# Optimization experiments

Hardware: AMD Instinct MI355X
Metric: run time of the kernel (lower is better)

Reference implementation:

```python
import jax, jax.numpy as jnp
import numpy as np

EMBED_DIM = 1024
NUM_HEADS = 16
HEAD_DIM = EMBED_DIM // NUM_HEADS
ROPE_BASE = 10000.0
NEG_INF = -1e9


def _rope_tables(T, dim, dtype=jnp.float32):
    inv_freq = 1.0 / (ROPE_BASE ** (jnp.arange(0, dim, 2, dtype=jnp.float32) / dim))
    t = jnp.arange(T, dtype=jnp.float32)
    freqs = jnp.einsum('t,f->tf', t, inv_freq)          # [T, dim/2]
    emb = jnp.concatenate([freqs, freqs], axis=-1)       # [T, dim]
    return jnp.cos(emb).astype(dtype), jnp.sin(emb).astype(dtype)


def _rotate_half(x):
    x1, x2 = jnp.split(x, 2, axis=-1)
    return jnp.concatenate([-x2, x1], axis=-1)


def setup_inputs() -> dict:
    key = jax.random.key(0)
    kx, kqkv, kout = jax.random.split(key, 3)
    B, T = 2, 2048
    x = jax.random.normal(kx, (B, T, EMBED_DIM), dtype=jnp.float32)
    # Dense kernels (no bias), glorot-ish scale
    w_qkv = jax.random.normal(kqkv, (EMBED_DIM, 3 * EMBED_DIM), dtype=jnp.float32) * (EMBED_DIM ** -0.5)
    w_out = jax.random.normal(kout, (EMBED_DIM, EMBED_DIM), dtype=jnp.float32) * (EMBED_DIM ** -0.5)
    return {"x": x, "w_qkv": w_qkv, "w_out": w_out}


def reference(x, w_qkv, w_out):
    B, T, _ = x.shape
    qkv = x @ w_qkv                                      # [B, T, 3E]
    q, k, v = jnp.split(qkv, 3, axis=-1)

    def split_heads(t):
        return t.reshape(B, T, NUM_HEADS, HEAD_DIM).transpose(0, 2, 1, 3)  # [B,H,T,D]

    q, k, v = split_heads(q), split_heads(k), split_heads(v)

    cos, sin = _rope_tables(T, HEAD_DIM, x.dtype)        # [T, D]
    cos = cos[None, None, :, :]
    sin = sin[None, None, :, :]
    q = q * cos + _rotate_half(q) * sin
    k = k * cos + _rotate_half(k) * sin

    scale = jnp.sqrt(jnp.asarray(HEAD_DIM, dtype=jnp.float32)).astype(x.dtype)
    scores = jnp.einsum('bhqd,bhkd->bhqk', q, k) / scale  # [B,H,T,T]
    causal = jnp.tril(jnp.ones((T, T), dtype=bool))[None, None, :, :]
    scores = jnp.where(causal, scores, jnp.asarray(NEG_INF, dtype=x.dtype))
    probs = jax.nn.softmax(scores, axis=-1)
    out = jnp.einsum('bhqk,bhkd->bhqd', probs, v)         # [B,H,T,D]
    out = out.transpose(0, 2, 1, 3).reshape(B, T, EMBED_DIM)
    return out @ w_out
```

## Files before the change

kernel.cpp:

```cpp
#include <hip/hip_runtime.h>
#include <hip/hip_bf16.h>
#include <cstdint>

#define DI __device__ __forceinline__

using u16x8  = __attribute__((ext_vector_type(8))) unsigned short;
using u32x4  = __attribute__((ext_vector_type(4))) unsigned int;
using bf16x8 = __attribute__((ext_vector_type(8))) __bf16;
using f32x4  = __attribute__((ext_vector_type(4))) float;


DI unsigned short f2bf(float f) {
  unsigned u = __builtin_bit_cast(unsigned, f);
  u += 0x7fffu + ((u >> 16) & 1u);
  return (unsigned short)(u >> 16);
}
DI float bf2f(unsigned short b) {
  unsigned u = (unsigned)b << 16;
  return __builtin_bit_cast(float, u);
}
DI unsigned cvt_pk_bf16(float lo, float hi) {
  unsigned r;
  asm("v_cvt_pk_bf16_f32 %0, %1, %2" : "=v"(r) : "v"(lo), "v"(hi));
  return r;
}
DI void permlane_swap32(unsigned& a, unsigned& b) {
  asm("v_permlane32_swap_b32 %0, %1" : "+v"(a), "+v"(b));
}
DI void permlane_swap16(unsigned& a, unsigned& b) {
  asm("v_permlane16_swap_b32 %0, %1" : "+v"(a), "+v"(b));
}

DI void gld_lds16(const void* g, void* l) {
  __builtin_amdgcn_global_load_lds(
      (const __attribute__((address_space(1))) void*)(uintptr_t)g,
      (__attribute__((address_space(3))) void*)(uint32_t)(uintptr_t)l,
      16, 0, 0);
}


__global__ __launch_bounds__(256) void cvt_bf16_kernel(const float* __restrict__ in,
                                                        unsigned short* __restrict__ out, int n) {
  int i = (blockIdx.x * 256 + threadIdx.x) * 8;
  if (i >= n) return;
  float4 v0 = *(const float4*)(in + i);
  float4 v1 = *(const float4*)(in + i + 4);
  u16x8 o;
  o[0] = f2bf(v0.x); o[1] = f2bf(v0.y); o[2] = f2bf(v0.z); o[3] = f2bf(v0.w);
  o[4] = f2bf(v1.x); o[5] = f2bf(v1.y); o[6] = f2bf(v1.z); o[7] = f2bf(v1.w);
  *(u16x8*)(out + i) = o;
}

__global__ __launch_bounds__(256) void transpose_cvt_kernel(const float* __restrict__ in,
                                                             unsigned short* __restrict__ out,
                                                             int K, int N) {
  __shared__ float tile[32][33];
  int n0 = blockIdx.x * 32, k0 = blockIdx.y * 32;
  int tx = threadIdx.x & 31, ty = threadIdx.x >> 5;
#pragma unroll
  for (int i = 0; i < 4; ++i)
    tile[ty * 4 + i][tx] = in[(size_t)(k0 + ty * 4 + i) * N + n0 + tx];
  __syncthreads();
#pragma unroll
  for (int i = 0; i < 4; ++i)
    out[(size_t)(n0 + ty * 4 + i) * K + k0 + tx] = f2bf(tile[tx][ty * 4 + i]);
}


template <int MODE>
__global__ __launch_bounds__(256)
void gemm_tn(const unsigned short* __restrict__ A, const unsigned short* __restrict__ B,
             unsigned short* __restrict__ q_out, unsigned short* __restrict__ k_out,
             unsigned short* __restrict__ v_out, float* __restrict__ c_out,
             int M, int N, int K) {
  __shared__ __align__(16) char smem[2][16384];
  const int tid = threadIdx.x;
  const int lane = tid & 63, wave = tid >> 6;
  const int wm = wave >> 1, wn = wave & 1;
  const int m0 = blockIdx.y << 7, n0 = blockIdx.x << 7;
  const int r15 = lane & 15, g4 = lane >> 4;

  const size_t Ks = (size_t)K;
  const unsigned short* aptr = A + (size_t)(m0 + wave * 16 + r15) * Ks + g4 * 8;
  const unsigned short* bptr = B + (size_t)(n0 + wave * 16 + r15) * Ks + g4 * 8;

  f32x4 acc[4][4] = {};
  const int NT = K >> 5;

  auto stage = [&](int buf, int kt) {
    const unsigned short* ak = aptr + kt * 32;
    const unsigned short* bk = bptr + kt * 32;
    char* sA = &smem[buf][0] + wave * 1024;
    char* sB = &smem[buf][8192] + wave * 1024;
    gld_lds16(ak, sA);
    gld_lds16(ak + 64 * Ks, sA + 4096);
    gld_lds16(bk, sB);
    gld_lds16(bk + 64 * Ks, sB + 4096);
  };

  stage(0, 0);
  __syncthreads();
  for (int kt = 0; kt < NT; ++kt) {
    int buf = kt & 1;
    if (kt + 1 < NT) stage(buf ^ 1, kt + 1);
    const char* base = &smem[buf][0];
    bf16x8 af[4], bfr[4];
#pragma unroll
    for (int mt = 0; mt < 4; ++mt)
      af[mt] = *(const bf16x8*)(base + ((wm * 4 + mt) * 64 + lane) * 16);
#pragma unroll
    for (int nt = 0; nt < 4; ++nt)
      bfr[nt] = *(const bf16x8*)(base + 8192 + ((wn * 4 + nt) * 64 + lane) * 16);
#pragma unroll
    for (int mt = 0; mt < 4; ++mt)
#pragma unroll
      for (int nt = 0; nt < 4; ++nt)
        acc[mt][nt] = __builtin_amdgcn_mfma_f32_16x16x32_bf16(af[mt], bfr[nt], acc[mt][nt], 0, 0, 0);
    __syncthreads();
  }

  const int gm0 = m0 + wm * 64, gn0 = n0 + wn * 64;
  if constexpr (MODE == 0) {
    const int region = gn0 >> 10;
    const int h = (gn0 & 1023) >> 6;
    if (region <= 1) {
      unsigned short* dst = (region == 0) ? q_out : k_out;
      const float qs = (region == 0) ? (0.125f * 1.44269504088896341f) : 1.0f;
#pragma unroll
      for (int mt = 0; mt < 4; ++mt) {
#pragma unroll
        for (int r = 0; r < 4; ++r) {
          int mrow = gm0 + mt * 16 + g4 * 4 + r;
          int b = mrow >> 11, t = mrow & 2047;
          unsigned short* rowp = dst + (((size_t)(b * 16 + h) * 2048 + t) << 6);
          float tf = (float)t;
#pragma unroll
          for (int nt = 0; nt < 2; ++nt) {
            int j = nt * 16 + r15;
            float invf = exp2f((float)j * -0.4152410118609203f);
            float ang = tf * invf;
            float sv, cv;
            sincosf(ang, &sv, &cv);
            float x1 = acc[mt][nt][r], x2 = acc[mt][nt + 2][r];
            rowp[j]      = f2bf((x1 * cv - x2 * sv) * qs);
            rowp[j + 32] = f2bf((x2 * cv + x1 * sv) * qs);
          }
        }
      }
    } else {
#pragma unroll
      for (int mt = 0; mt < 4; ++mt)
#pragma unroll
        for (int r = 0; r < 4; ++r) {
          int mrow = gm0 + mt * 16 + g4 * 4 + r;
          int b = mrow >> 11, t = mrow & 2047;
          unsigned short* colp = v_out + ((size_t)(b * 16 + h) * 64) * 2048 + t;
#pragma unroll
          for (int nt = 0; nt < 4; ++nt)
            colp[(size_t)(nt * 16 + r15) * 2048] = f2bf(acc[mt][nt][r]);
        }
    }
  } else {
#pragma unroll
    for (int mt = 0; mt < 4; ++mt)
#pragma unroll
      for (int r = 0; r < 4; ++r) {
        int mrow = gm0 + mt * 16 + g4 * 4 + r;
        float* rowp = c_out + (size_t)mrow * N + gn0;
#pragma unroll
        for (int nt = 0; nt < 4; ++nt)
          rowp[nt * 16 + r15] = acc[mt][nt][r];
      }
  }
}


__global__ __launch_bounds__(256)
void attn_fused(const unsigned short* __restrict__ qb, const unsigned short* __restrict__ kb,
                const unsigned short* __restrict__ vt, unsigned short* __restrict__ attno,
                unsigned short* __restrict__ pO, float* __restrict__ pml) {
  __shared__ __align__(16) char ksm[2][8192];
  __shared__ __align__(16) char vsm[2][8192];

  const int tid = threadIdx.x, lane = tid & 63, wave = tid >> 6;
  const int r15 = lane & 15, g4 = lane >> 4;

  const int wg = blockIdx.x;
  const int swz = (wg & 7) * 96 + (wg >> 3);
  const int bh = swz / 24;
  const int rb = swz % 24;
  int J, c; bool multi;
  if (rb < 8) { J = rb; c = 0; multi = false; }
  else { int rr = rb - 8; J = 8 + (rr >> 1); c = rr & 1; multi = true; }
  const int ntw = 2 * J + 2;
  const int ktmid = J + 1;
  const int kt0 = (multi && c) ? ktmid : 0;
  const int ktN = multi ? (c ? ntw : ktmid) : ntw;
  const int q0 = J << 7;
  const int q0w = q0 + wave * 32;

  const size_t hb = (size_t)bh * 2048 * 64;
  const unsigned short* Qp = qb + hb;
  const unsigned short* Kp = kb + hb;
  const unsigned short* Vp = vt + hb;

  bf16x8 qf[2][2];
#pragma unroll
  for (int mq = 0; mq < 2; ++mq)
#pragma unroll
    for (int kc = 0; kc < 2; ++kc)
      qf[mq][kc] = *(const bf16x8*)(Qp + (size_t)(q0w + mq * 16 + r15) * 64 + kc * 32 + g4 * 8);

  f32x4 o[2][4] = {};
  float mr[2] = {-INFINITY, -INFINITY};
  float lr[2] = {0.f, 0.f};

  auto stage = [&](int buf, int kt) {
    const int kv0 = kt << 6;
#pragma unroll
    for (int i = 0; i < 2; ++i) {
      int f = wave * 2 + i;
      int nt = f >> 1, kc = f & 1;
      gld_lds16(Kp + (size_t)(kv0 + nt * 16 + r15) * 64 + kc * 32 + g4 * 8, &ksm[buf][f * 1024]);
      gld_lds16(Vp + (size_t)(nt * 16 + r15) * 2048 + kv0 + kc * 32 + g4 * 8, &vsm[buf][f * 1024]);
    }
  };

  auto process = [&](int buf, int kv0, bool mask) {
    bf16x8 kf[8];
#pragma unroll
    for (int i = 0; i < 8; ++i)
      kf[i] = *(const bf16x8*)(&ksm[buf][i * 1024] + lane * 16);

    f32x4 s[4][2] = {};
    __builtin_amdgcn_s_setprio(1);
#pragma unroll
    for (int nt = 0; nt < 4; ++nt)
#pragma unroll
      for (int kc = 0; kc < 2; ++kc) {
        s[nt][0] = __builtin_amdgcn_mfma_f32_16x16x32_bf16(kf[nt * 2 + kc], qf[0][kc], s[nt][0], 0, 0, 0);
        s[nt][1] = __builtin_amdgcn_mfma_f32_16x16x32_bf16(kf[nt * 2 + kc], qf[1][kc], s[nt][1], 0, 0, 0);
      }
    __builtin_amdgcn_s_setprio(0);

    if (mask) {
#pragma unroll
      for (int nt = 0; nt < 4; ++nt)
#pragma unroll
        for (int mq = 0; mq < 2; ++mq)
#pragma unroll
          for (int r = 0; r < 4; ++r)
            if (kv0 + nt * 16 + g4 * 4 + r > q0w + mq * 16 + r15) s[nt][mq][r] = -1e9f;
    }

    bf16x8 pa[2][2];
#pragma unroll
    for (int mq = 0; mq < 2; ++mq) {
      float m0 = fmaxf(fmaxf(s[0][mq][0], s[0][mq][1]), fmaxf(s[0][mq][2], s[0][mq][3]));
      float m1 = fmaxf(fmaxf(s[1][mq][0], s[1][mq][1]), fmaxf(s[1][mq][2], s[1][mq][3]));
      float m2 = fmaxf(fmaxf(s[2][mq][0], s[2][mq][1]), fmaxf(s[2][mq][2], s[2][mq][3]));
      float m3 = fmaxf(fmaxf(s[3][mq][0], s[3][mq][1]), fmaxf(s[3][mq][2], s[3][mq][3]));
      float mx = fmaxf(fmaxf(m0, m1), fmaxf(m2, m3));
      mx = fmaxf(mx, __shfl_xor(mx, 16));
      mx = fmaxf(mx, __shfl_xor(mx, 32));
      float mnew = fmaxf(mr[mq], mx);
      float fsc = exp2f(mr[mq] - mnew);
      mr[mq] = mnew;
      float t0 = 0.f, t1 = 0.f, t2 = 0.f, t3 = 0.f;
#pragma unroll
      for (int nt = 0; nt < 4; ++nt) {
        float p0 = exp2f(s[nt][mq][0] - mnew);
        float p1 = exp2f(s[nt][mq][1] - mnew);
        float p2 = exp2f(s[nt][mq][2] - mnew);
        float p3 = exp2f(s[nt][mq][3] - mnew);
        s[nt][mq][0] = p0; s[nt][mq][1] = p1; s[nt][mq][2] = p2; s[nt][mq][3] = p3;
        if (nt == 0) t0 = (p0 + p1) + (p2 + p3);
        if (nt == 1) t1 = (p0 + p1) + (p2 + p3);
        if (nt == 2) t2 = (p0 + p1) + (p2 + p3);
        if (nt == 3) t3 = (p0 + p1) + (p2 + p3);
      }
      float ps = (t0 + t1) + (t2 + t3);
      ps += __shfl_xor(ps, 16);
      ps += __shfl_xor(ps, 32);
      lr[mq] = lr[mq] * fsc + ps;
#pragma unroll
      for (int r = 0; r < 4; ++r) {
        float fr = __shfl(fsc, (g4 << 2) + r);
#pragma unroll
        for (int dt = 0; dt < 4; ++dt) o[mq][dt][r] *= fr;
      }
      unsigned p32[4][2];
#pragma unroll
      for (int nt = 0; nt < 4; ++nt) {
        p32[nt][0] = cvt_pk_bf16(s[nt][mq][0], s[nt][mq][1]);
        p32[nt][1] = cvt_pk_bf16(s[nt][mq][2], s[nt][mq][3]);
      }
#pragma unroll
      for (int kc = 0; kc < 2; ++kc) {
        u32x4 w;
#pragma unroll
        for (int pi = 0; pi < 2; ++pi) {
          unsigned a = p32[2 * kc][pi], b = p32[2 * kc + 1][pi];
          permlane_swap32(a, b);
          permlane_swap16(a, b);
          w[pi] = a;
          w[2 + pi] = b;
        }
        pa[mq][kc] = __builtin_bit_cast(bf16x8, w);
      }
    }

    bf16x8 vf[8];
#pragma unroll
    for (int i = 0; i < 8; ++i)
      vf[i] = *(const bf16x8*)(&vsm[buf][i * 1024] + lane * 16);

    __builtin_amdgcn_s_setprio(1);
#pragma unroll
    for (int kc = 0; kc < 2; ++kc)
#pragma unroll
      for (int dt = 0; dt < 4; ++dt) {
        o[0][dt] = __builtin_amdgcn_mfma_f32_16x16x32_bf16(pa[0][kc], vf[dt * 2 + kc], o[0][dt], 0, 0, 0);
        o[1][dt] = __builtin_amdgcn_mfma_f32_16x16x32_bf16(pa[1][kc], vf[dt * 2 + kc], o[1][dt], 0, 0, 0);
      }
    __builtin_amdgcn_s_setprio(0);
  };

  int buf = 0;
  stage(0, kt0);
  __syncthreads();
  for (int kt = kt0; kt < ktN; ++kt) {
    if (kt + 1 < ktN) stage(buf ^ 1, kt + 1);
    const int kv0 = kt << 6;
    if (kv0 <= q0w + 31)
      process(buf, kv0, kv0 + 63 > q0w);
    __syncthreads();
    buf ^= 1;
  }

  if (!multi) {
    const int b = bh >> 4, h = bh & 15;
#pragma unroll
    for (int mq = 0; mq < 2; ++mq) {
      float inv = 1.f / lr[mq];
#pragma unroll
      for (int r = 0; r < 4; ++r) {
        float ir = __shfl(inv, (g4 << 2) + r);
        int q = q0w + mq * 16 + g4 * 4 + r;
        unsigned short* rowp = attno + (size_t)(b * 2048 + q) * 1024 + h * 64;
#pragma unroll
        for (int dt = 0; dt < 4; ++dt)
          rowp[dt * 16 + r15] = f2bf(o[mq][dt][r] * ir);
      }
    }
  } else {
    const int sidx = (bh * 8 + (J - 8)) * 2 + c;
    unsigned short* po = pO + (size_t)sidx * 8192 + wave * 32 * 64;
#pragma unroll
    for (int mq = 0; mq < 2; ++mq)
#pragma unroll
      for (int r = 0; r < 4; ++r)
#pragma unroll
        for (int dt = 0; dt < 4; ++dt)
          po[(mq * 16 + g4 * 4 + r) * 64 + dt * 16 + r15] = f2bf(o[mq][dt][r]);
    if (g4 == 0) {
      float* pm = pml + sidx * 256 + wave * 32;
#pragma unroll
      for (int mq = 0; mq < 2; ++mq) {
        pm[mq * 16 + r15] = mr[mq];
        pm[128 + mq * 16 + r15] = lr[mq];
      }
    }
  }
}

__global__ __launch_bounds__(256)
void attn_combine(const unsigned short* __restrict__ pO, const float* __restrict__ pml,
                  unsigned short* __restrict__ attno) {
  const int bx = blockIdx.x;
  const int bh = bx >> 3, Jrel = bx & 7, J = 8 + Jrel;
  const int t = threadIdx.x;
  const int row = t >> 1;
  const int dh = (t & 1) << 5;
  const int s0i = (bh * 8 + Jrel) * 2;
  const float* pm0 = pml + s0i * 256;
  const float* pm1 = pm0 + 256;
  float m0 = pm0[row], l0 = pm0[128 + row];
  float m1 = pm1[row], l1 = pm1[128 + row];
  float mg = fmaxf(m0, m1);
  float s0 = exp2f(m0 - mg), s1 = exp2f(m1 - mg);
  float inv = 1.f / (l0 * s0 + l1 * s1);
  s0 *= inv; s1 *= inv;
  const unsigned short* o0 = pO + (size_t)s0i * 8192 + row * 64 + dh;
  const unsigned short* o1 = o0 + 8192;
  const int b = bh >> 4, h = bh & 15;
  const int q = J * 128 + row;
  unsigned short* dst = attno + (size_t)(b * 2048 + q) * 1024 + h * 64 + dh;
#pragma unroll
  for (int dd = 0; dd < 32; dd += 8) {
    u16x8 a = *(const u16x8*)(o0 + dd);
    u16x8 bq = *(const u16x8*)(o1 + dd);
    u16x8 ov;
#pragma unroll
    for (int e = 0; e < 8; ++e)
      ov[e] = f2bf(bf2f(a[e]) * s0 + bf2f(bq[e]) * s1);
    *(u16x8*)(dst + dd) = ov;
  }
}


extern "C" void kernel_launch(void* const* d_in, const int* in_sizes, int n_in,
                              void* d_out, int out_size, void* d_ws, size_t ws_size,
                              hipStream_t stream) {
  const float* x     = (const float*)d_in[0];
  const float* w_qkv = (const float*)d_in[1];
  const float* w_out = (const float*)d_in[2];
  float* out = (float*)d_out;

  char* ws = (char*)d_ws;
  unsigned short* xb  = (unsigned short*)(ws);
  unsigned short* wqT = (unsigned short*)(ws + (8u << 20));
  unsigned short* woT = (unsigned short*)(ws + (14u << 20));
  unsigned short* qb  = (unsigned short*)(ws + (16u << 20));
  unsigned short* kb  = (unsigned short*)(ws + (24u << 20));
  unsigned short* vt  = (unsigned short*)(ws + (32u << 20));
  unsigned short* ao  = (unsigned short*)(ws + (40u << 20));
  unsigned short* pO  = xb;
  float*          pml = (float*)wqT;

  cvt_bf16_kernel<<<2048, 256, 0, stream>>>(x, xb, 4096 * 1024);
  transpose_cvt_kernel<<<dim3(96, 32), 256, 0, stream>>>(w_qkv, wqT, 1024, 3072);
  transpose_cvt_kernel<<<dim3(32, 32), 256, 0, stream>>>(w_out, woT, 1024, 1024);
  gemm_tn<0><<<dim3(24, 32), 256, 0, stream>>>(xb, wqT, qb, kb, vt, nullptr, 4096, 3072, 1024);
  attn_fused<<<768, 256, 0, stream>>>(qb, kb, vt, ao, pO, pml);
  attn_combine<<<256, 256, 0, stream>>>(pO, pml, ao);
  gemm_tn<1><<<dim3(8, 32), 256, 0, stream>>>(ao, woT, nullptr, nullptr, nullptr, out, 4096, 1024, 1024);
}
```

Before: 173.5 us.

## Add XCD-aware block mapping, LDS-staged V store, lazy softmax rescale

```diff
diff --git a/kernel.cpp b/kernel.cpp
--- a/kernel.cpp
+++ b/kernel.cpp
@@ -77,7 +77,14 @@
   const int tid = threadIdx.x;
   const int lane = tid & 63, wave = tid >> 6;
   const int wm = wave >> 1, wn = wave & 1;
-  const int m0 = blockIdx.y << 7, n0 = blockIdx.x << 7;
+
+  constexpr int BANDW = (MODE == 0) ? 3 : 1;
+  const int id = blockIdx.x;
+  const int xcd = id & 7, rr = id >> 3;
+  const int bx = xcd * BANDW + rr % BANDW;
+  const int by = rr / BANDW;
+  const int m0 = by << 7, n0 = bx << 7;
+
   const int r15 = lane & 15, g4 = lane >> 4;
 
   const size_t Ks = (size_t)K;
@@ -148,17 +155,28 @@
         }
       }
     } else {
-#pragma unroll
-      for (int mt = 0; mt < 4; ++mt)
-#pragma unroll
-        for (int r = 0; r < 4; ++r) {
-          int mrow = gm0 + mt * 16 + g4 * 4 + r;
-          int b = mrow >> 11, t = mrow & 2047;
-          unsigned short* colp = v_out + ((size_t)(b * 16 + h) * 64) * 2048 + t;
-#pragma unroll
-          for (int nt = 0; nt < 4; ++nt)
-            colp[(size_t)(nt * 16 + r15) * 2048] = f2bf(acc[mt][nt][r]);
+      const int b = gm0 >> 11, t0 = gm0 & 2047;
+      unsigned short* vhead = v_out + ((size_t)(b * 16 + h) * 64) * 2048;
+      short* tb = (short*)(&smem[0][0] + wave * 8192);
+#pragma unroll
+      for (int p = 0; p < 2; ++p) {
+#pragma unroll
+        for (int np = 0; np < 2; ++np)
+#pragma unroll
+          for (int mt = 0; mt < 4; ++mt)
+#pragma unroll
+            for (int pr = 0; pr < 2; ++pr) {
+              unsigned pk = cvt_pk_bf16(acc[mt][2 * p + np][2 * pr], acc[mt][2 * p + np][2 * pr + 1]);
+              *(unsigned*)(tb + (np * 16 + r15) * 72 + mt * 16 + g4 * 4 + pr * 2) = pk;
+            }
+#pragma unroll
+        for (int cc = 0; cc < 4; ++cc) {
+          int dl = cc * 8 + (lane >> 3);
+          int tc = (lane & 7) * 8;
+          u16x8 vv = *(const u16x8*)(tb + dl * 72 + tc);
+          *(u16x8*)(vhead + (size_t)(p * 32 + dl) * 2048 + t0 + tc) = vv;
         }
+      }
     }
   } else {
 #pragma unroll
@@ -174,6 +192,10 @@
   }
 }
 
+
+__device__ const int RBMAP[24] = {7, 23, 20, 21, 18, 19, 17, 5,
+                                  22, 6, 16, 12, 13, 14, 15, 10,
+                                  0, 1, 2, 3, 8, 9, 4, 11};
 
 __global__ __launch_bounds__(256)
 void attn_fused(const unsigned short* __restrict__ qb, const unsigned short* __restrict__ kb,
@@ -186,9 +208,9 @@
   const int r15 = lane & 15, g4 = lane >> 4;
 
   const int wg = blockIdx.x;
-  const int swz = (wg & 7) * 96 + (wg >> 3);
-  const int bh = swz / 24;
-  const int rb = swz % 24;
+  const int qq = wg >> 3;
+  const int bh = (wg & 7) * 4 + qq / 24;
+  const int rb = RBMAP[qq % 24];
   int J, c; bool multi;
   if (rb < 8) { J = rb; c = 0; multi = false; }
   else { int rr = rb - 8; J = 8 + (rr >> 1); c = rr & 1; multi = true; }
@@ -263,9 +285,21 @@
       float mx = fmaxf(fmaxf(m0, m1), fmaxf(m2, m3));
       mx = fmaxf(mx, __shfl_xor(mx, 16));
       mx = fmaxf(mx, __shfl_xor(mx, 32));
-      float mnew = fmaxf(mr[mq], mx);
-      float fsc = exp2f(mr[mq] - mnew);
-      mr[mq] = mnew;
+      float mnew;
+      if (!__all(mx <= mr[mq] + 8.f)) {
+        mnew = fmaxf(mr[mq], mx);
+        float fsc = exp2f(mr[mq] - mnew);
+        mr[mq] = mnew;
+        lr[mq] *= fsc;
+#pragma unroll
+        for (int r = 0; r < 4; ++r) {
+          float fr = __shfl(fsc, (g4 << 2) + r);
+#pragma unroll
+          for (int dt = 0; dt < 4; ++dt) o[mq][dt][r] *= fr;
+        }
+      } else {
+        mnew = mr[mq];
+      }
       float t0 = 0.f, t1 = 0.f, t2 = 0.f, t3 = 0.f;
 #pragma unroll
       for (int nt = 0; nt < 4; ++nt) {
@@ -282,13 +316,7 @@
       float ps = (t0 + t1) + (t2 + t3);
       ps += __shfl_xor(ps, 16);
       ps += __shfl_xor(ps, 32);
-      lr[mq] = lr[mq] * fsc + ps;
-#pragma unroll
-      for (int r = 0; r < 4; ++r) {
-        float fr = __shfl(fsc, (g4 << 2) + r);
-#pragma unroll
-        for (int dt = 0; dt < 4; ++dt) o[mq][dt][r] *= fr;
-      }
+      lr[mq] += ps;
       unsigned p32[4][2];
 #pragma unroll
       for (int nt = 0; nt < 4; ++nt) {
@@ -431,8 +459,8 @@
   cvt_bf16_kernel<<<2048, 256, 0, stream>>>(x, xb, 4096 * 1024);
   transpose_cvt_kernel<<<dim3(96, 32), 256, 0, stream>>>(w_qkv, wqT, 1024, 3072);
   transpose_cvt_kernel<<<dim3(32, 32), 256, 0, stream>>>(w_out, woT, 1024, 1024);
-  gemm_tn<0><<<dim3(24, 32), 256, 0, stream>>>(xb, wqT, qb, kb, vt, nullptr, 4096, 3072, 1024);
+  gemm_tn<0><<<768, 256, 0, stream>>>(xb, wqT, qb, kb, vt, nullptr, 4096, 3072, 1024);
   attn_fused<<<768, 256, 0, stream>>>(qb, kb, vt, ao, pO, pml);
   attn_combine<<<256, 256, 0, stream>>>(pO, pml, ao);
-  gemm_tn<1><<<dim3(8, 32), 256, 0, stream>>>(ao, woT, nullptr, nullptr, nullptr, out, 4096, 1024, 1024);
-}
+  gemm_tn<1><<<256, 256, 0, stream>>>(ao, woT, nullptr, nullptr, nullptr, out, 4096, 1024, 1024);
+}
```

After: 159.1 us. 8.3% less time.
